# Performance work log

Hardware: AMD Instinct MI355X
Metric: run time of the kernel (lower is better)

The kernel has to match this reference:

```python
import jax, jax.numpy as jnp
import numpy as np


def setup_inputs() -> dict:
    key = jax.random.key(0)
    k1, k2, k3 = jax.random.split(key, 3)
    b, n, d, f = 16, 2048, 256, 256
    features = jax.random.normal(k1, (b, n, d), dtype=jnp.float32)
    # dense adjacency; row-normalize like MeanAggregator's normalized A
    A = jax.random.uniform(k2, (b, n, n), dtype=jnp.float32)
    A = A / jnp.sum(A, axis=-1, keepdims=True)
    weight = jax.random.normal(k3, (2 * d, f), dtype=jnp.float32) * (1.0 / np.sqrt(2 * d))
    bias = jnp.zeros((f,), dtype=jnp.float32)
    return {"features": features, "A": A, "weight": weight, "bias": bias}


def reference(features, A, weight, bias):
    # agg = A @ features  (MeanAggregator: row-normalized adjacency)
    agg = jnp.einsum('bnm,bmd->bnd', A, features)  # [b,n,d]
    d = features.shape[-1]
    # split-weight GEMM instead of materializing concat:
    # [feat, agg] @ W == feat @ W[:d] + agg @ W[d:]
    out = (jnp.einsum('bnd,df->bnf', features, weight[:d])
           + jnp.einsum('bnd,df->bnf', agg, weight[d:])
           + bias)
    return jax.nn.relu(out)
```

## Files before the change

### kernel.cpp

```cpp
#include <hip/hip_runtime.h>

typedef __attribute__((ext_vector_type(8))) short bf16x8;
typedef __attribute__((ext_vector_type(4))) float f32x4;

__device__ __forceinline__ unsigned short f2bf(float f) {
    unsigned int u = __builtin_bit_cast(unsigned int, f);
    unsigned int r = (u + 0x7FFFu + ((u >> 16) & 1u)) >> 16;
    return (unsigned short)r;
}
__device__ __forceinline__ unsigned int pkbf(float lo, float hi) {
    unsigned int ul = __builtin_bit_cast(unsigned int, lo) + 0x8000u;
    unsigned int uh = __builtin_bit_cast(unsigned int, hi) + 0x8000u;
    return (uh & 0xFFFF0000u) | (ul >> 16);
}

__device__ __forceinline__ void gll16(const void* g, void* l) {
    __builtin_amdgcn_global_load_lds(
        (const __attribute__((address_space(1))) void*)g,
        (__attribute__((address_space(3))) void*)l, 16, 0, 0);
}

__global__ __launch_bounds__(256) void transpose_cvt_kernel(
    const float* __restrict__ src, unsigned short* __restrict__ dstT,
    unsigned short* __restrict__ dstS, int R, int C)
{
    __shared__ float tile[64][65];
    const int b = blockIdx.z;
    const float* s = src + (size_t)b * R * C;
    const int r0 = blockIdx.x * 64, c0 = blockIdx.y * 64;
    const int t = threadIdx.x;
    const int r = t >> 2, cg = (t & 3) * 16;

    float v[16];
    const float4* p = reinterpret_cast<const float4*>(s + (size_t)(r0 + r) * C + c0 + cg);
#pragma unroll
    for (int i = 0; i < 4; ++i) {
        float4 q = p[i];
        v[4 * i + 0] = q.x; v[4 * i + 1] = q.y; v[4 * i + 2] = q.z; v[4 * i + 3] = q.w;
    }
#pragma unroll
    for (int i = 0; i < 16; ++i) tile[r][cg + i] = v[i];

    if (dstS) {
        unsigned int w[8];
#pragma unroll
        for (int i = 0; i < 8; ++i)
            w[i] = (unsigned)f2bf(v[2 * i]) | ((unsigned)f2bf(v[2 * i + 1]) << 16);
        unsigned int* d = reinterpret_cast<unsigned int*>(
            dstS + (size_t)b * R * C + (size_t)(r0 + r) * C + c0 + cg);
        *reinterpret_cast<uint4*>(d)     = make_uint4(w[0], w[1], w[2], w[3]);
        *reinterpret_cast<uint4*>(d + 4) = make_uint4(w[4], w[5], w[6], w[7]);
    }

    __syncthreads();

    const int cl = t >> 2, rg = (t & 3) * 16;
    unsigned int w[8];
#pragma unroll
    for (int i = 0; i < 8; ++i) {
        unsigned short lo = f2bf(tile[rg + 2 * i][cl]);
        unsigned short hi = f2bf(tile[rg + 2 * i + 1][cl]);
        w[i] = (unsigned)lo | ((unsigned)hi << 16);
    }
    unsigned int* d = reinterpret_cast<unsigned int*>(
        dstT + (size_t)b * R * C + (size_t)(c0 + cl) * R + r0 + rg);
    *reinterpret_cast<uint4*>(d)     = make_uint4(w[0], w[1], w[2], w[3]);
    *reinterpret_cast<uint4*>(d + 4) = make_uint4(w[4], w[5], w[6], w[7]);
}

__global__ __launch_bounds__(512, 4) void k1_agg_gemm(
    const float* __restrict__ A, const unsigned short* __restrict__ Ft,
    unsigned short* __restrict__ agg0, unsigned short* __restrict__ agg1)
{
    __shared__ short Ab[128][64];
    __shared__ short Bb[256][64];

    const int tid = threadIdx.x;
    const int lane = tid & 63, wid = tid >> 6;
    const int wr = wid >> 2, wc = wid & 3;
    const int lo = lane & 15, hi = lane >> 4;

    const int bid = blockIdx.x;
    const int wg = ((bid & 7) << 6) | (bid >> 3);
    const int batch = wg >> 5;
    const int ks    = (wg >> 4) & 1;
    const int mt    = wg & 15;

    const float* Abase = A + ((size_t)batch * 2048 + (size_t)mt * 128) * 2048 + (size_t)ks * 1024;
    const unsigned short* Fbase = Ft + (size_t)batch * 256 * 2048 + (size_t)ks * 1024;

    const int arow = tid >> 2;
    const int acg  = tid & 3;

    f32x4 acc[4][4];
#pragma unroll
    for (int m = 0; m < 4; ++m)
#pragma unroll
        for (int n = 0; n < 4; ++n) acc[m][n] = (f32x4){0.f, 0.f, 0.f, 0.f};

    for (int t = 0; t < 16; ++t) {
        const int k0 = t * 64;
        const float4* p = reinterpret_cast<const float4*>(
            Abase + (size_t)arow * 2048 + k0 + acg * 16);
        float4 q0 = p[0], q1 = p[1], q2 = p[2], q3 = p[3];
#pragma unroll
        for (int it = 0; it < 4; ++it) {
            int si = it * 512 + tid;
            int row = si >> 3, slot = si & 7;
            const unsigned short* g = Fbase + (size_t)row * 2048 + k0 + ((slot ^ (row & 7)) << 3);
            short* l = &Bb[0][0] + (size_t)(it * 512 + (wid << 6)) * 8;
            gll16(g, l);
        }
        unsigned int w0 = pkbf(q0.x, q0.y), w1 = pkbf(q0.z, q0.w);
        unsigned int w2 = pkbf(q1.x, q1.y), w3 = pkbf(q1.z, q1.w);
        unsigned int w4 = pkbf(q2.x, q2.y), w5 = pkbf(q2.z, q2.w);
        unsigned int w6 = pkbf(q3.x, q3.y), w7 = pkbf(q3.z, q3.w);
        {
            int slin = acg * 2;
            int off0 = arow * 64 + (((slin    ) ^ (arow & 7)) << 3);
            int off1 = arow * 64 + (((slin + 1) ^ (arow & 7)) << 3);
            *reinterpret_cast<uint4*>(&Ab[0][0] + off0) = make_uint4(w0, w1, w2, w3);
            *reinterpret_cast<uint4*>(&Ab[0][0] + off1) = make_uint4(w4, w5, w6, w7);
        }
        __syncthreads();

#pragma unroll
        for (int kk = 0; kk < 2; ++kk) {
            bf16x8 af[4], bfv[4];
#pragma unroll
            for (int m = 0; m < 4; ++m) {
                int row = wr * 64 + m * 16 + lo;
                int off = row * 64 + (((kk * 4 + hi) ^ (row & 7)) << 3);
                af[m] = *reinterpret_cast<const bf16x8*>(&Ab[0][0] + off);
            }
#pragma unroll
            for (int n = 0; n < 4; ++n) {
                int row = wc * 64 + n * 16 + lo;
                int off = row * 64 + (((kk * 4 + hi) ^ (row & 7)) << 3);
                bfv[n] = *reinterpret_cast<const bf16x8*>(&Bb[0][0] + off);
            }
#pragma unroll
            for (int m = 0; m < 4; ++m)
#pragma unroll
                for (int n = 0; n < 4; ++n)
                    acc[m][n] = __builtin_amdgcn_mfma_f32_16x16x32_bf16(af[m], bfv[n], acc[m][n], 0, 0, 0);
        }
        __syncthreads();
    }

    unsigned short* obase = (ks ? agg1 : agg0)
        + ((size_t)batch * 2048 + (size_t)mt * 128) * 256;
#pragma unroll
    for (int m = 0; m < 4; ++m) {
#pragma unroll
        for (int n = 0; n < 4; ++n) {
            int col = wc * 64 + n * 16 + lo;
#pragma unroll
            for (int j = 0; j < 4; ++j) {
                int row = wr * 64 + m * 16 + hi * 4 + j;
                obase[(size_t)row * 256 + col] = f2bf(acc[m][n][j]);
            }
        }
    }
}

__global__ __launch_bounds__(256, 2) void k2_out_gemm(
    const unsigned short* __restrict__ Fb, const unsigned short* __restrict__ agg0,
    const unsigned short* __restrict__ agg1, const unsigned short* __restrict__ Wt,
    const float* __restrict__ bias, float* __restrict__ out)
{
    __shared__ short Ab[64][64];
    __shared__ short Bb[256][64];

    const int tid = threadIdx.x;
    const int lane = tid & 63, wid = tid >> 6;
    const int wc = wid;
    const int lo = lane & 15, hi = lane >> 4;
    const int m0 = blockIdx.x * 64;

    f32x4 acc[4][4];
#pragma unroll
    for (int m = 0; m < 4; ++m)
#pragma unroll
        for (int n = 0; n < 4; ++n) acc[m][n] = (f32x4){0.f, 0.f, 0.f, 0.f};

    for (int t = 0; t < 12; ++t) {
        const int k0 = t * 64;
        const unsigned short* asrc = (k0 < 256) ? Fb : (k0 < 512 ? agg0 : agg1);
        const int ak = k0 & 255;
#pragma unroll
        for (int it = 0; it < 2; ++it) {
            int si = it * 256 + tid;
            int row = si >> 3, slot = si & 7;
            const unsigned short* g = asrc + (size_t)(m0 + row) * 256 + ak + ((slot ^ (row & 7)) << 3);
            short* l = &Ab[0][0] + (size_t)(it * 256 + (wid << 6)) * 8;
            gll16(g, l);
        }
        const int bk = (k0 < 512) ? k0 : k0 - 256;
#pragma unroll
        for (int it = 0; it < 8; ++it) {
            int si = it * 256 + tid;
            int row = si >> 3, slot = si & 7;
            const unsigned short* g = Wt + (size_t)row * 512 + bk + ((slot ^ (row & 7)) << 3);
            short* l = &Bb[0][0] + (size_t)(it * 256 + (wid << 6)) * 8;
            gll16(g, l);
        }
        __syncthreads();

#pragma unroll
        for (int kk = 0; kk < 2; ++kk) {
            bf16x8 af[4], bfv[4];
#pragma unroll
            for (int m = 0; m < 4; ++m) {
                int row = m * 16 + lo;
                int off = row * 64 + (((kk * 4 + hi) ^ (row & 7)) << 3);
                af[m] = *reinterpret_cast<const bf16x8*>(&Ab[0][0] + off);
            }
#pragma unroll
            for (int n = 0; n < 4; ++n) {
                int row = wc * 64 + n * 16 + lo;
                int off = row * 64 + (((kk * 4 + hi) ^ (row & 7)) << 3);
                bfv[n] = *reinterpret_cast<const bf16x8*>(&Bb[0][0] + off);
            }
#pragma unroll
            for (int m = 0; m < 4; ++m)
#pragma unroll
                for (int n = 0; n < 4; ++n)
                    acc[m][n] = __builtin_amdgcn_mfma_f32_16x16x32_bf16(af[m], bfv[n], acc[m][n], 0, 0, 0);
        }
        __syncthreads();
    }

    float bv[4];
#pragma unroll
    for (int n = 0; n < 4; ++n) bv[n] = bias[wc * 64 + n * 16 + lo];

#pragma unroll
    for (int m = 0; m < 4; ++m) {
#pragma unroll
        for (int n = 0; n < 4; ++n) {
            int col = wc * 64 + n * 16 + lo;
#pragma unroll
            for (int j = 0; j < 4; ++j) {
                int row = m0 + m * 16 + hi * 4 + j;
                float v = acc[m][n][j] + bv[n];
                out[(size_t)row * 256 + col] = fmaxf(v, 0.f);
            }
        }
    }
}

extern "C" void kernel_launch(void* const* d_in, const int* in_sizes, int n_in,
                              void* d_out, int out_size, void* d_ws, size_t ws_size,
                              hipStream_t stream) {
    const float* features = (const float*)d_in[0];
    const float* A        = (const float*)d_in[1];
    const float* weight   = (const float*)d_in[2];
    const float* bias     = (const float*)d_in[3];
    float* out = (float*)d_out;

    const size_t F_ELEMS = (size_t)16 * 2048 * 256;
    const size_t FT_B   = F_ELEMS * 2;
    const size_t FB_B   = F_ELEMS * 2;
    const size_t WT_B   = (size_t)256 * 512 * 2;
    const size_t AGG_B  = F_ELEMS * 2;
    if (ws_size < FT_B + FB_B + WT_B + 2 * AGG_B) return;

    char* ws = (char*)d_ws;
    unsigned short* Ft   = (unsigned short*)ws;
    unsigned short* Fb   = (unsigned short*)(ws + FT_B);
    unsigned short* Wt   = (unsigned short*)(ws + FT_B + FB_B);
    unsigned short* agg0 = (unsigned short*)(ws + FT_B + FB_B + WT_B);
    unsigned short* agg1 = (unsigned short*)(ws + FT_B + FB_B + WT_B + AGG_B);

    dim3 gF(2048 / 64, 256 / 64, 16);
    transpose_cvt_kernel<<<gF, 256, 0, stream>>>(features, Ft, Fb, 2048, 256);
    dim3 gW(512 / 64, 256 / 64, 1);
    transpose_cvt_kernel<<<gW, 256, 0, stream>>>(weight, Wt, nullptr, 512, 256);

    k1_agg_gemm<<<512, 512, 0, stream>>>(A, Ft, agg0, agg1);

    k2_out_gemm<<<512, 256, 0, stream>>>(Fb, agg0, agg1, Wt, bias, out);
}
```

Baseline: 126.4 us.

## Reassociate to A@(F@W2) and fuse the output GEMM into the aggregation epilogue

```diff
diff --git a/kernel.cpp b/kernel.cpp
--- a/kernel.cpp
+++ b/kernel.cpp
@@ -12,6 +12,10 @@
     unsigned int ul = __builtin_bit_cast(unsigned int, lo) + 0x8000u;
     unsigned int uh = __builtin_bit_cast(unsigned int, hi) + 0x8000u;
     return (uh & 0xFFFF0000u) | (ul >> 16);
+}
+__device__ __forceinline__ float bf2f(unsigned short u) {
+    unsigned int x = ((unsigned int)u) << 16;
+    return __builtin_bit_cast(float, x);
 }
 
 __device__ __forceinline__ void gll16(const void* g, void* l) {
@@ -68,12 +72,133 @@
     *reinterpret_cast<uint4*>(d + 4) = make_uint4(w[4], w[5], w[6], w[7]);
 }
 
-__global__ __launch_bounds__(512, 4) void k1_agg_gemm(
-    const float* __restrict__ A, const unsigned short* __restrict__ Ft,
-    unsigned short* __restrict__ agg0, unsigned short* __restrict__ agg1)
+__global__ __launch_bounds__(256, 2) void kpre_gemm(
+    const float* __restrict__ F, const unsigned short* __restrict__ Wt,
+    const float* __restrict__ bias, unsigned short* __restrict__ H,
+    unsigned short* __restrict__ Gt)
 {
-    __shared__ short Ab[128][64];
-    __shared__ short Bb[256][64];
+    __shared__ __align__(16) short Fb[64 * 256];
+    __shared__ __align__(16) short Wb[256 * 64];
+
+    const int tid = threadIdx.x;
+    const int lane = tid & 63, wid = tid >> 6;
+    const int lo = lane & 15, hi = lane >> 4;
+    const int rb = blockIdx.x;
+    const int batch = rb >> 5;
+    const int mb = (rb & 31) * 64;
+    const size_t m0g = (size_t)rb * 64;
+
+    {
+        const int frow = tid >> 2, fq = tid & 3;
+        const float* fp = F + (m0g + frow) * 256 + fq * 64;
+#pragma unroll
+        for (int g = 0; g < 2; ++g) {
+            float4 q[8];
+#pragma unroll
+            for (int i = 0; i < 8; ++i)
+                q[i] = reinterpret_cast<const float4*>(fp)[g * 8 + i];
+#pragma unroll
+            for (int j = 0; j < 4; ++j) {
+                unsigned int w0 = pkbf(q[2*j].x,   q[2*j].y);
+                unsigned int w1 = pkbf(q[2*j].z,   q[2*j].w);
+                unsigned int w2 = pkbf(q[2*j+1].x, q[2*j+1].y);
+                unsigned int w3 = pkbf(q[2*j+1].z, q[2*j+1].w);
+                int slot = fq * 8 + g * 4 + j;
+                int off = frow * 256 + ((slot ^ (frow & 7)) << 3);
+                *reinterpret_cast<uint4*>(&Fb[off]) = make_uint4(w0, w1, w2, w3);
+            }
+        }
+    }
+
+    f32x4 acc[4][4];
+
+#pragma unroll
+    for (int pass = 0; pass < 2; ++pass) {
+#pragma unroll
+        for (int m = 0; m < 4; ++m)
+#pragma unroll
+            for (int n = 0; n < 4; ++n) acc[m][n] = (f32x4){0.f, 0.f, 0.f, 0.f};
+
+        for (int kt = 0; kt < 4; ++kt) {
+            const int kbase = pass * 256 + kt * 64;
+#pragma unroll
+            for (int it = 0; it < 8; ++it) {
+                int si = it * 256 + tid;
+                int row = si >> 3, slot = si & 7;
+                const unsigned short* g = Wt + (size_t)row * 512 + kbase + ((slot ^ (row & 7)) << 3);
+                gll16(g, Wb + (size_t)si * 8);
+            }
+            __syncthreads();
+
+#pragma unroll
+            for (int kk = 0; kk < 2; ++kk) {
+                bf16x8 af[4], bw[4];
+#pragma unroll
+                for (int m = 0; m < 4; ++m) {
+                    int row = m * 16 + lo;
+                    int slot = kt * 8 + kk * 4 + hi;
+                    af[m] = *reinterpret_cast<const bf16x8*>(&Fb[row * 256 + ((slot ^ (row & 7)) << 3)]);
+                }
+#pragma unroll
+                for (int n = 0; n < 4; ++n) {
+                    int row = wid * 64 + n * 16 + lo;
+                    bw[n] = *reinterpret_cast<const bf16x8*>(&Wb[row * 64 + (((kk * 4 + hi) ^ (row & 7)) << 3)]);
+                }
+#pragma unroll
+                for (int m = 0; m < 4; ++m)
+#pragma unroll
+                    for (int n = 0; n < 4; ++n)
+                        acc[m][n] = __builtin_amdgcn_mfma_f32_16x16x32_bf16(af[m], bw[n], acc[m][n], 0, 0, 0);
+            }
+            __syncthreads();
+        }
+
+        if (pass == 0) {
+            float bv[4];
+#pragma unroll
+            for (int n = 0; n < 4; ++n) bv[n] = bias[wid * 64 + n * 16 + lo];
+            unsigned short* Hb = H + m0g * 256;
+#pragma unroll
+            for (int m = 0; m < 4; ++m)
+#pragma unroll
+                for (int n = 0; n < 4; ++n)
+#pragma unroll
+                    for (int j = 0; j < 4; ++j) {
+                        int row = m * 16 + hi * 4 + j;
+                        int col = wid * 64 + n * 16 + lo;
+                        Hb[(size_t)row * 256 + col] = f2bf(acc[m][n][j] + bv[n]);
+                    }
+        } else {
+            short* T = Wb + wid * 4096;
+#pragma unroll
+            for (int m = 0; m < 4; ++m)
+#pragma unroll
+                for (int n = 0; n < 4; ++n)
+#pragma unroll
+                    for (int j = 0; j < 4; ++j) {
+                        int gr = m * 16 + hi * 4 + j;
+                        int gc = n * 16 + lo;
+                        int slot = gr >> 3, e = gr & 7;
+                        T[gc * 64 + ((slot ^ (gc & 7)) << 3) + e] = f2bf(acc[m][n][j]);
+                    }
+            unsigned short* Gb = Gt + ((size_t)batch * 256 + wid * 64) * 2048 + mb;
+#pragma unroll
+            for (int i = 0; i < 8; ++i) {
+                int f = i * 8 + (lane >> 3);
+                int s = lane & 7;
+                bf16x8 v = *reinterpret_cast<const bf16x8*>(&T[f * 64 + ((s ^ (f & 7)) << 3)]);
+                *reinterpret_cast<bf16x8*>(Gb + (size_t)f * 2048 + s * 8) = v;
+            }
+        }
+    }
+}
+
+__global__ __launch_bounds__(512, 2) void kmain_gemm(
+    const float* __restrict__ A, const unsigned short* __restrict__ Gt,
+    const unsigned short* __restrict__ H, float* __restrict__ out)
+{
+    __shared__ __align__(16) short Ab[128 * 64];
+    __shared__ __align__(16) short Bb[256 * 64];
 
     const int tid = threadIdx.x;
     const int lane = tid & 63, wid = tid >> 6;
@@ -81,13 +206,12 @@
     const int lo = lane & 15, hi = lane >> 4;
 
     const int bid = blockIdx.x;
-    const int wg = ((bid & 7) << 6) | (bid >> 3);
-    const int batch = wg >> 5;
-    const int ks    = (wg >> 4) & 1;
+    const int wg = ((bid & 7) << 5) | (bid >> 3);
+    const int batch = wg >> 4;
     const int mt    = wg & 15;
 
-    const float* Abase = A + ((size_t)batch * 2048 + (size_t)mt * 128) * 2048 + (size_t)ks * 1024;
-    const unsigned short* Fbase = Ft + (size_t)batch * 256 * 2048 + (size_t)ks * 1024;
+    const float* Abase = A + ((size_t)batch * 2048 + (size_t)mt * 128) * 2048;
+    const unsigned short* Gbase = Gt + (size_t)batch * 256 * 2048;
 
     const int arow = tid >> 2;
     const int acg  = tid & 3;
@@ -98,31 +222,39 @@
 #pragma unroll
         for (int n = 0; n < 4; ++n) acc[m][n] = (f32x4){0.f, 0.f, 0.f, 0.f};
 
-    for (int t = 0; t < 16; ++t) {
-        const int k0 = t * 64;
+    float4 qa[4];
+    auto load_A = [&](int k0) {
         const float4* p = reinterpret_cast<const float4*>(
             Abase + (size_t)arow * 2048 + k0 + acg * 16);
-        float4 q0 = p[0], q1 = p[1], q2 = p[2], q3 = p[3];
+#pragma unroll
+        for (int i = 0; i < 4; ++i) qa[i] = p[i];
+    };
+
+    load_A(0);
+
+    for (int t = 0; t < 32; ++t) {
+        const int k0 = t * 64;
 #pragma unroll
         for (int it = 0; it < 4; ++it) {
             int si = it * 512 + tid;
             int row = si >> 3, slot = si & 7;
-            const unsigned short* g = Fbase + (size_t)row * 2048 + k0 + ((slot ^ (row & 7)) << 3);
-            short* l = &Bb[0][0] + (size_t)(it * 512 + (wid << 6)) * 8;
-            gll16(g, l);
-        }
-        unsigned int w0 = pkbf(q0.x, q0.y), w1 = pkbf(q0.z, q0.w);
-        unsigned int w2 = pkbf(q1.x, q1.y), w3 = pkbf(q1.z, q1.w);
-        unsigned int w4 = pkbf(q2.x, q2.y), w5 = pkbf(q2.z, q2.w);
-        unsigned int w6 = pkbf(q3.x, q3.y), w7 = pkbf(q3.z, q3.w);
+            const unsigned short* g = Gbase + (size_t)row * 2048 + k0 + ((slot ^ (row & 7)) << 3);
+            gll16(g, Bb + (size_t)si * 8);
+        }
         {
+            unsigned int w0 = pkbf(qa[0].x, qa[0].y), w1 = pkbf(qa[0].z, qa[0].w);
+            unsigned int w2 = pkbf(qa[1].x, qa[1].y), w3 = pkbf(qa[1].z, qa[1].w);
+            unsigned int w4 = pkbf(qa[2].x, qa[2].y), w5 = pkbf(qa[2].z, qa[2].w);
+            unsigned int w6 = pkbf(qa[3].x, qa[3].y), w7 = pkbf(qa[3].z, qa[3].w);
             int slin = acg * 2;
             int off0 = arow * 64 + (((slin    ) ^ (arow & 7)) << 3);
             int off1 = arow * 64 + (((slin + 1) ^ (arow & 7)) << 3);
-            *reinterpret_cast<uint4*>(&Ab[0][0] + off0) = make_uint4(w0, w1, w2, w3);
-            *reinterpret_cast<uint4*>(&Ab[0][0] + off1) = make_uint4(w4, w5, w6, w7);
+            *reinterpret_cast<uint4*>(&Ab[off0]) = make_uint4(w0, w1, w2, w3);
+            *reinterpret_cast<uint4*>(&Ab[off1]) = make_uint4(w4, w5, w6, w7);
         }
         __syncthreads();
+
+        if (t + 1 < 32) load_A((t + 1) * 64);
 
 #pragma unroll
         for (int kk = 0; kk < 2; ++kk) {
@@ -130,14 +262,12 @@
 #pragma unroll
             for (int m = 0; m < 4; ++m) {
                 int row = wr * 64 + m * 16 + lo;
-                int off = row * 64 + (((kk * 4 + hi) ^ (row & 7)) << 3);
-                af[m] = *reinterpret_cast<const bf16x8*>(&Ab[0][0] + off);
+                af[m] = *reinterpret_cast<const bf16x8*>(&Ab[row * 64 + (((kk * 4 + hi) ^ (row & 7)) << 3)]);
             }
 #pragma unroll
             for (int n = 0; n < 4; ++n) {
                 int row = wc * 64 + n * 16 + lo;
-                int off = row * 64 + (((kk * 4 + hi) ^ (row & 7)) << 3);
-                bfv[n] = *reinterpret_cast<const bf16x8*>(&Bb[0][0] + off);
+                bfv[n] = *reinterpret_cast<const bf16x8*>(&Bb[row * 64 + (((kk * 4 + hi) ^ (row & 7)) << 3)]);
             }
 #pragma unroll
             for (int m = 0; m < 4; ++m)
@@ -148,8 +278,9 @@
         __syncthreads();
     }
 
-    unsigned short* obase = (ks ? agg1 : agg0)
-        + ((size_t)batch * 2048 + (size_t)mt * 128) * 256;
+    const size_t rowbase = (size_t)batch * 2048 + (size_t)mt * 128;
+    const unsigned short* Hb = H + rowbase * 256;
+    float* obase = out + rowbase * 256;
 #pragma unroll
     for (int m = 0; m < 4; ++m) {
 #pragma unroll
@@ -158,93 +289,8 @@
 #pragma unroll
             for (int j = 0; j < 4; ++j) {
                 int row = wr * 64 + m * 16 + hi * 4 + j;
-                obase[(size_t)row * 256 + col] = f2bf(acc[m][n][j]);
-            }
-        }
-    }
-}
-
-__global__ __launch_bounds__(256, 2) void k2_out_gemm(
-    const unsigned short* __restrict__ Fb, const unsigned short* __restrict__ agg0,
-    const unsigned short* __restrict__ agg1, const unsigned short* __restrict__ Wt,
-    const float* __restrict__ bias, float* __restrict__ out)
-{
-    __shared__ short Ab[64][64];
-    __shared__ short Bb[256][64];
-
-    const int tid = threadIdx.x;
-    const int lane = tid & 63, wid = tid >> 6;
-    const int wc = wid;
-    const int lo = lane & 15, hi = lane >> 4;
-    const int m0 = blockIdx.x * 64;
-
-    f32x4 acc[4][4];
-#pragma unroll
-    for (int m = 0; m < 4; ++m)
-#pragma unroll
-        for (int n = 0; n < 4; ++n) acc[m][n] = (f32x4){0.f, 0.f, 0.f, 0.f};
-
-    for (int t = 0; t < 12; ++t) {
-        const int k0 = t * 64;
-        const unsigned short* asrc = (k0 < 256) ? Fb : (k0 < 512 ? agg0 : agg1);
-        const int ak = k0 & 255;
-#pragma unroll
-        for (int it = 0; it < 2; ++it) {
-            int si = it * 256 + tid;
-            int row = si >> 3, slot = si & 7;
-            const unsigned short* g = asrc + (size_t)(m0 + row) * 256 + ak + ((slot ^ (row & 7)) << 3);
-            short* l = &Ab[0][0] + (size_t)(it * 256 + (wid << 6)) * 8;
-            gll16(g, l);
-        }
-        const int bk = (k0 < 512) ? k0 : k0 - 256;
-#pragma unroll
-        for (int it = 0; it < 8; ++it) {
-            int si = it * 256 + tid;
-            int row = si >> 3, slot = si & 7;
-            const unsigned short* g = Wt + (size_t)row * 512 + bk + ((slot ^ (row & 7)) << 3);
-            short* l = &Bb[0][0] + (size_t)(it * 256 + (wid << 6)) * 8;
-            gll16(g, l);
-        }
-        __syncthreads();
-
-#pragma unroll
-        for (int kk = 0; kk < 2; ++kk) {
-            bf16x8 af[4], bfv[4];
-#pragma unroll
-            for (int m = 0; m < 4; ++m) {
-                int row = m * 16 + lo;
-                int off = row * 64 + (((kk * 4 + hi) ^ (row & 7)) << 3);
-                af[m] = *reinterpret_cast<const bf16x8*>(&Ab[0][0] + off);
-            }
-#pragma unroll
-            for (int n = 0; n < 4; ++n) {
-                int row = wc * 64 + n * 16 + lo;
-                int off = row * 64 + (((kk * 4 + hi) ^ (row & 7)) << 3);
-                bfv[n] = *reinterpret_cast<const bf16x8*>(&Bb[0][0] + off);
-            }
-#pragma unroll
-            for (int m = 0; m < 4; ++m)
-#pragma unroll
-                for (int n = 0; n < 4; ++n)
-                    acc[m][n] = __builtin_amdgcn_mfma_f32_16x16x32_bf16(af[m], bfv[n], acc[m][n], 0, 0, 0);
-        }
-        __syncthreads();
-    }
-
-    float bv[4];
-#pragma unroll
-    for (int n = 0; n < 4; ++n) bv[n] = bias[wc * 64 + n * 16 + lo];
-
-#pragma unroll
-    for (int m = 0; m < 4; ++m) {
-#pragma unroll
-        for (int n = 0; n < 4; ++n) {
-            int col = wc * 64 + n * 16 + lo;
-#pragma unroll
-            for (int j = 0; j < 4; ++j) {
-                int row = m0 + m * 16 + hi * 4 + j;
-                float v = acc[m][n][j] + bv[n];
-                out[(size_t)row * 256 + col] = fmaxf(v, 0.f);
+                float v = acc[m][n][j] + bf2f(Hb[(size_t)row * 256 + col]);
+                obase[(size_t)row * 256 + col] = fmaxf(v, 0.f);
             }
         }
     }
@@ -259,26 +305,20 @@
     const float* bias     = (const float*)d_in[3];
     float* out = (float*)d_out;
 
-    const size_t F_ELEMS = (size_t)16 * 2048 * 256;
-    const size_t FT_B   = F_ELEMS * 2;
-    const size_t FB_B   = F_ELEMS * 2;
-    const size_t WT_B   = (size_t)256 * 512 * 2;
-    const size_t AGG_B  = F_ELEMS * 2;
-    if (ws_size < FT_B + FB_B + WT_B + 2 * AGG_B) return;
+    const size_t WT_B = (size_t)256 * 512 * 2;
+    const size_t H_B  = (size_t)32768 * 256 * 2;
+    const size_t GT_B = (size_t)16 * 256 * 2048 * 2;
+    if (ws_size < WT_B + H_B + GT_B) return;
 
     char* ws = (char*)d_ws;
-    unsigned short* Ft   = (unsigned short*)ws;
-    unsigned short* Fb   = (unsigned short*)(ws + FT_B);
-    unsigned short* Wt   = (unsigned short*)(ws + FT_B + FB_B);
-    unsigned short* agg0 = (unsigned short*)(ws + FT_B + FB_B + WT_B);
-    unsigned short* agg1 = (unsigned short*)(ws + FT_B + FB_B + WT_B + AGG_B);
-
-    dim3 gF(2048 / 64, 256 / 64, 16);
-    transpose_cvt_kernel<<<gF, 256, 0, stream>>>(features, Ft, Fb, 2048, 256);
+    unsigned short* Wt = (unsigned short*)ws;
+    unsigned short* H  = (unsigned short*)(ws + WT_B);
+    unsigned short* Gt = (unsigned short*)(ws + WT_B + H_B);
+
     dim3 gW(512 / 64, 256 / 64, 1);
     transpose_cvt_kernel<<<gW, 256, 0, stream>>>(weight, Wt, nullptr, 512, 256);
 
-    k1_agg_gemm<<<512, 512, 0, stream>>>(A, Ft, agg0, agg1);
-
-    k2_out_gemm<<<512, 256, 0, stream>>>(Fb, agg0, agg1, Wt, bias, out);
-}
+    kpre_gemm<<<512, 256, 0, stream>>>(features, Wt, bias, H, Gt);
+
+    kmain_gemm<<<256, 512, 0, stream>>>(A, Gt, H, out);
+}
```

Measured after the change: 115.4 us. 1.1x faster.
